# Performance work log

Measured on AMD Instinct MI355X. Metric: run time of the kernel, lower is better.

The kernel has to match this reference:

```python
import jax, jax.numpy as jnp
import numpy as np

EPS = 1e-6  # torch.nn.CosineSimilarity eps


def setup_inputs() -> dict:
    key = jax.random.key(0)
    k1, k2, k3, k4 = jax.random.split(key, 4)
    B, S, I, H, P = 16, 512, 512, 512, 16
    hidden = jax.random.normal(k1, (B, S, I), dtype=jnp.float32)
    # per-prototype linear weights (no bias); torch Linear stores (out, in)
    W1 = jax.random.normal(k2, (P, H, I), dtype=jnp.float32) / np.sqrt(I)
    W2 = jax.random.normal(k3, (P, H, H), dtype=jnp.float32) / np.sqrt(H)
    protos = jax.random.normal(k4, (P, H), dtype=jnp.float32)  # torch.randn(1,H) per proto
    return {"hidden": hidden, "W1": W1, "W2": W2, "protos": protos}


def reference(hidden, W1, W2, protos):
    # Batched version of the per-prototype loop:
    # layer1: ReLU(hidden @ W1[p].T) -> [B,S,P,H]
    h1 = jax.nn.relu(jnp.einsum("bsi,phi->bsph", hidden, W1))
    # layer2: ReLU(h1 @ W2[p].T) -> [B,S,P,H]
    h2 = jax.nn.relu(jnp.einsum("bsph,pgh->bspg", h1, W2))
    # cosine similarity along feature dim vs. each prototype vector
    dot = jnp.einsum("bsph,ph->bsp", h2, protos)
    xn = jnp.maximum(jnp.linalg.norm(h2, axis=-1), EPS)          # [B,S,P]
    pn = jnp.maximum(jnp.linalg.norm(protos, axis=-1), EPS)      # [P]
    cos_scores = dot / (xn * pn)                                  # [B,S,P]
    return cos_scores
```

## Files before the change

### kernel.cpp

```cpp
#include <hip/hip_runtime.h>
#include <hip/hip_bf16.h>

#define R_TOT 8192
#define DIM   512
#define NP    16
#define EPSV  1e-6f

typedef __bf16 bf16x8 __attribute__((ext_vector_type(8)));
typedef float  f32x4  __attribute__((ext_vector_type(4)));

__device__ __forceinline__ unsigned int f2bf(float f) {
  unsigned int u = __float_as_uint(f);
  return (u + 0x7FFFu + ((u >> 16) & 1u)) >> 16;
}
__device__ __forceinline__ unsigned int pack2(float a, float b) {
  return f2bf(a) | (f2bf(b) << 16);
}

__global__ void cvt_x_kernel(const float* __restrict__ X, unsigned short* __restrict__ Xb) {
  int t   = blockIdx.x * 256 + threadIdx.x;
  int row = t >> 6;
  int c   = t & 63;
  const float4* src = (const float4*)(X + (size_t)row * DIM + c * 8);
  float4 f0 = src[0], f1 = src[1];
  uint4 o;
  o.x = pack2(f0.x, f0.y);
  o.y = pack2(f0.z, f0.w);
  o.z = pack2(f1.x, f1.y);
  o.w = pack2(f1.z, f1.w);
  *(uint4*)(Xb + (size_t)row * DIM + 8 * (c ^ (row & 7))) = o;
}

__global__ void pack_w_kernel(const float* __restrict__ W, unsigned short* __restrict__ Wp) {
  int t  = blockIdx.x * 256 + threadIdx.x;
  int l  = t & 63;
  int kk = (t >> 6) & 15;
  int mt = (t >> 10) & 31;
  int p  = t >> 15;
  int row = mt * 16 + (l & 15);
  int k0  = 32 * kk + 8 * (l >> 4);
  const float4* s = (const float4*)(W + ((size_t)p * DIM + row) * DIM + k0);
  float4 f0 = s[0], f1 = s[1];
  uint4 o;
  o.x = pack2(f0.x, f0.y);
  o.y = pack2(f0.z, f0.w);
  o.z = pack2(f1.x, f1.y);
  o.w = pack2(f1.z, f1.w);
  *(uint4*)(Wp + (size_t)t * 8) = o;
}

__global__ void proto_norm_kernel(const float* __restrict__ protos, float* __restrict__ pn) {
  int p = blockIdx.x;
  int l = threadIdx.x;
  float ss = 0.f;
  #pragma unroll
  for (int k = 0; k < DIM / 64; ++k) {
    float v = protos[p * DIM + k * 64 + l];
    ss += v * v;
  }
  #pragma unroll
  for (int m = 32; m >= 1; m >>= 1) ss += __shfl_xor(ss, m, 64);
  if (l == 0) pn[p] = fmaxf(sqrtf(ss), EPSV);
}

__device__ __forceinline__ void gemm_stage(const unsigned short* tile,
                                           const unsigned short* __restrict__ Wpk,
                                           f32x4 acc[4][4],
                                           int l, int l15, int q) {
  for (int kk = 0; kk < 16; ++kk) {
    bf16x8 a[4], b[4];
    #pragma unroll
    for (int mi = 0; mi < 4; ++mi)
      a[mi] = *(const bf16x8*)(Wpk + (size_t)mi * 8192 + kk * 512 + l * 8);
    #pragma unroll
    for (int nt = 0; nt < 4; ++nt) {
      int token = nt * 16 + l15;
      int boff  = (64 * kk + 16 * q) ^ ((token & 7) << 4);
      b[nt] = *(const bf16x8*)((const char*)tile + token * 1024 + boff);
    }
    __builtin_amdgcn_s_setprio(1);
    #pragma unroll
    for (int mi = 0; mi < 4; ++mi)
      #pragma unroll
      for (int nt = 0; nt < 4; ++nt)
        acc[mi][nt] = __builtin_amdgcn_mfma_f32_16x16x32_bf16(a[mi], b[nt], acc[mi][nt], 0, 0, 0);
    __builtin_amdgcn_s_setprio(0);
  }
}

__global__ __launch_bounds__(512, 3) void fused_kernel(
    const unsigned short* __restrict__ Xb,
    const unsigned short* __restrict__ W1p,
    const unsigned short* __restrict__ W2p,
    const float* __restrict__ protos,
    const float* __restrict__ pn,
    float* __restrict__ out) {
  __shared__ unsigned short tile[64 * DIM];
  __shared__ float red[8][64][2];

  const int raw = blockIdx.x;
  const int bid = (raw & 7) * 256 + (raw >> 3);
  const int p   = bid >> 7;
  const int r0  = (bid & 127) << 6;
  const int tid = threadIdx.x;
  const int w   = tid >> 6;
  const int l   = tid & 63;
  const int l15 = l & 15;
  const int q   = l >> 4;

  {
    const uint4* g = (const uint4*)(Xb + (size_t)r0 * DIM);
    uint4* s = (uint4*)tile;
    #pragma unroll
    for (int it = 0; it < 8; ++it) s[tid + it * 512] = g[tid + it * 512];
  }
  __syncthreads();

  f32x4 acc[4][4];
  #pragma unroll
  for (int mi = 0; mi < 4; ++mi)
    #pragma unroll
    for (int nt = 0; nt < 4; ++nt) acc[mi][nt] = (f32x4){0.f, 0.f, 0.f, 0.f};

  gemm_stage(tile, W1p + ((size_t)p * 32 + 4 * w) * 8192, acc, l, l15, q);

  __syncthreads();

  #pragma unroll
  for (int mi = 0; mi < 4; ++mi)
    #pragma unroll
    for (int nt = 0; nt < 4; ++nt) {
      int token = nt * 16 + l15;
      int featb = ((4 * w + mi) * 16 + q * 4) * 2;
      uint2 pk;
      pk.x = pack2(fmaxf(acc[mi][nt][0], 0.f), fmaxf(acc[mi][nt][1], 0.f));
      pk.y = pack2(fmaxf(acc[mi][nt][2], 0.f), fmaxf(acc[mi][nt][3], 0.f));
      *(uint2*)((char*)tile + token * 1024 + (featb ^ ((token & 7) << 4))) = pk;
    }
  __syncthreads();

  #pragma unroll
  for (int mi = 0; mi < 4; ++mi)
    #pragma unroll
    for (int nt = 0; nt < 4; ++nt) acc[mi][nt] = (f32x4){0.f, 0.f, 0.f, 0.f};

  gemm_stage(tile, W2p + ((size_t)p * 32 + 4 * w) * 8192, acc, l, l15, q);

  float4 pv[4];
  #pragma unroll
  for (int mi = 0; mi < 4; ++mi)
    pv[mi] = *(const float4*)(protos + p * DIM + (4 * w + mi) * 16 + q * 4);

  #pragma unroll
  for (int nt = 0; nt < 4; ++nt) {
    float d = 0.f, ssq = 0.f;
    #pragma unroll
    for (int mi = 0; mi < 4; ++mi)
      #pragma unroll
      for (int j = 0; j < 4; ++j) {
        float h = fmaxf(acc[mi][nt][j], 0.f);
        d   += h * ((const float*)&pv[mi])[j];
        ssq += h * h;
      }
    d   += __shfl_xor(d, 16, 64);
    d   += __shfl_xor(d, 32, 64);
    ssq += __shfl_xor(ssq, 16, 64);
    ssq += __shfl_xor(ssq, 32, 64);
    if (q == 0) {
      red[w][nt * 16 + l15][0] = d;
      red[w][nt * 16 + l15][1] = ssq;
    }
  }
  __syncthreads();

  if (tid < 64) {
    float d = 0.f, ssq = 0.f;
    #pragma unroll
    for (int ww = 0; ww < 8; ++ww) {
      d   += red[ww][tid][0];
      ssq += red[ww][tid][1];
    }
    float xn = fmaxf(sqrtf(ssq), EPSV);
    out[(size_t)(r0 + tid) * NP + p] = d / (xn * pn[p]);
  }
}

extern "C" void kernel_launch(void* const* d_in, const int* in_sizes, int n_in,
                              void* d_out, int out_size, void* d_ws, size_t ws_size,
                              hipStream_t stream) {
  const float* X      = (const float*)d_in[0];
  const float* W1     = (const float*)d_in[1];
  const float* W2     = (const float*)d_in[2];
  const float* protos = (const float*)d_in[3];
  float* out = (float*)d_out;

  unsigned short* Xb  = (unsigned short*)d_ws;
  unsigned short* W1p = Xb  + (size_t)R_TOT * DIM;
  unsigned short* W2p = W1p + (size_t)NP * DIM * DIM;
  float* pn = (float*)(W2p + (size_t)NP * DIM * DIM);

  cvt_x_kernel<<<2048, 256, 0, stream>>>(X, Xb);
  pack_w_kernel<<<2048, 256, 0, stream>>>(W1, W1p);
  pack_w_kernel<<<2048, 256, 0, stream>>>(W2, W2p);
  proto_norm_kernel<<<NP, 64, 0, stream>>>(protos, pn);
  fused_kernel<<<2048, 512, 0, stream>>>(Xb, W1p, W2p, protos, pn, out);
}
```

Measured before the change: 150.1 us.

## Double-buffer GEMM operand loads with sched barriers and relax occupancy bound

The per-k GEMM loop is replaced by a fully unrolled, register double-buffered pipeline. Operands for step k+1 (global weight fragments and LDS activation fragments) are loaded while the MFMAs for step k issue, with sched_barrier fences pinning that order. Launch bounds drop from 3 to 2 blocks per CU so the extra operand registers fit. The aim is to hide global and LDS load latency behind matrix math, at the cost of lower occupancy and losing the setprio hints.

Result: no change. 148.6 us (-1.0%).

```diff
diff --git a/kernel.cpp b/kernel.cpp
--- a/kernel.cpp
+++ b/kernel.cpp
@@ -63,32 +63,50 @@
   if (l == 0) pn[p] = fmaxf(sqrtf(ss), EPSV);
 }
 
+#define LOAD_SLOT(aS, bS, KK)                                                          \
+  {                                                                                    \
+    _Pragma("unroll")                                                                  \
+    for (int mi = 0; mi < 4; ++mi)                                                     \
+      aS[mi] = *(const bf16x8*)(Wpk + (size_t)mi * 8192 + (KK) * 512 + l * 8);         \
+    _Pragma("unroll")                                                                  \
+    for (int nt = 0; nt < 4; ++nt) {                                                   \
+      int token = nt * 16 + l15;                                                       \
+      int boff  = (64 * (KK) + 16 * q) ^ ((token & 7) << 4);                           \
+      bS[nt] = *(const bf16x8*)(tbase + token * 1024 + boff);                          \
+    }                                                                                  \
+  }
+
+#define MFMA_SLOT(aS, bS)                                                              \
+  {                                                                                    \
+    _Pragma("unroll")                                                                  \
+    for (int mi = 0; mi < 4; ++mi)                                                     \
+      _Pragma("unroll")                                                                \
+      for (int nt = 0; nt < 4; ++nt)                                                   \
+        acc[mi][nt] = __builtin_amdgcn_mfma_f32_16x16x32_bf16(aS[mi], bS[nt],          \
+                                                              acc[mi][nt], 0, 0, 0);  \
+  }
+
 __device__ __forceinline__ void gemm_stage(const unsigned short* tile,
                                            const unsigned short* __restrict__ Wpk,
                                            f32x4 acc[4][4],
                                            int l, int l15, int q) {
-  for (int kk = 0; kk < 16; ++kk) {
-    bf16x8 a[4], b[4];
-    #pragma unroll
-    for (int mi = 0; mi < 4; ++mi)
-      a[mi] = *(const bf16x8*)(Wpk + (size_t)mi * 8192 + kk * 512 + l * 8);
-    #pragma unroll
-    for (int nt = 0; nt < 4; ++nt) {
-      int token = nt * 16 + l15;
-      int boff  = (64 * kk + 16 * q) ^ ((token & 7) << 4);
-      b[nt] = *(const bf16x8*)((const char*)tile + token * 1024 + boff);
-    }
-    __builtin_amdgcn_s_setprio(1);
-    #pragma unroll
-    for (int mi = 0; mi < 4; ++mi)
-      #pragma unroll
-      for (int nt = 0; nt < 4; ++nt)
-        acc[mi][nt] = __builtin_amdgcn_mfma_f32_16x16x32_bf16(a[mi], b[nt], acc[mi][nt], 0, 0, 0);
-    __builtin_amdgcn_s_setprio(0);
-  }
-}
-
-__global__ __launch_bounds__(512, 3) void fused_kernel(
+  const char* tbase = (const char*)tile;
+  bf16x8 a0[4], a1[4], b0[4], b1[4];
+  LOAD_SLOT(a0, b0, 0)
+  #pragma unroll
+  for (int kk = 0; kk < 16; kk += 2) {
+    LOAD_SLOT(a1, b1, kk + 1)
+    __builtin_amdgcn_sched_barrier(0);
+    MFMA_SLOT(a0, b0)
+    __builtin_amdgcn_sched_barrier(0);
+    if (kk + 2 < 16) LOAD_SLOT(a0, b0, kk + 2)
+    __builtin_amdgcn_sched_barrier(0);
+    MFMA_SLOT(a1, b1)
+    __builtin_amdgcn_sched_barrier(0);
+  }
+}
+
+__global__ __launch_bounds__(512, 2) void fused_kernel(
     const unsigned short* __restrict__ Xb,
     const unsigned short* __restrict__ W1p,
     const unsigned short* __restrict__ W2p,
```
